# Kernel optimization log

Hardware: AMD Instinct MI355X
Metric: run time of the kernel (lower is better)

The kernel has to match this reference:

```python
import jax, jax.numpy as jnp
import numpy as np

N, F, P, O, E = 20000, 8, 12, 32, 320000


def setup_inputs() -> dict:
    key = jax.random.key(0)
    ks = jax.random.split(key, 18)
    g = lambda k, shape: (jax.random.normal(k, shape, jnp.float32) * 0.1)
    x = jax.random.normal(ks[0], (N, F, P), jnp.float32)
    edge_index = jax.random.randint(ks[1], (2, E), 0, N, dtype=jnp.int32)
    return {
        "x": x,
        "edge_index": edge_index,
        # GCNConv weights/biases for update (z), reset (r), candidate (h) gates
        "Wz": g(ks[2], (F, O)), "bz": g(ks[3], (O,)),
        "Wr": g(ks[4], (F, O)), "br": g(ks[5], (O,)),
        "Wh": g(ks[6], (F, O)), "bh": g(ks[7], (O,)),
        # GRU linear layers (torch.nn.Linear: y = x @ W.T + b), in=2*O, out=O
        "lz_w": g(ks[8], (O, 2 * O)), "lz_b": g(ks[9], (O,)),
        "lr_w": g(ks[10], (O, 2 * O)), "lr_b": g(ks[11], (O,)),
        "lh_w": g(ks[12], (O, 2 * O)), "lh_b": g(ks[13], (O,)),
        # temporal attention logits over periods
        "att": g(ks[14], (P,)),
        # final Linear(32 -> window_size)
        "out_w": g(ks[15], (P, O)), "out_b": g(ks[16], (P,)),
    }


def reference(x, edge_index, Wz, bz, Wr, br, Wh, bh,
              lz_w, lz_b, lr_w, lr_b, lh_w, lh_b, att, out_w, out_b):
    n = x.shape[0]
    # gcn_norm with self-loops: norm_e = d^-1/2[src] * d^-1/2[dst]
    loop = jnp.arange(n, dtype=edge_index.dtype)
    src = jnp.concatenate([edge_index[0], loop])
    dst = jnp.concatenate([edge_index[1], loop])
    deg = jax.ops.segment_sum(jnp.ones(src.shape[0], x.dtype), dst, num_segments=n)
    dinv = jnp.where(deg > 0, deg ** -0.5, 0.0)
    norm = dinv[src] * dinv[dst]  # [E+n]

    def gcn(xp, W, b):
        # xp: [n, P, F] -> [n, P, O]; GCNConv: D^-1/2 (A+I) D^-1/2 (X W) + b
        h = jnp.einsum('npf,fo->npo', xp, W)
        msg = h[src] * norm[:, None, None]  # [E+n, P, O]
        return jax.ops.segment_sum(msg, dst, num_segments=n) + b

    xp = jnp.transpose(x, (0, 2, 1))  # [n, P, F]
    # A3TGCN does NOT carry H across periods (H stays initial zeros), so all
    # periods are independent GRU steps from H = 0 and can be batched.
    H = jnp.zeros(xp.shape[:2] + (O,), x.dtype)
    Z = jax.nn.sigmoid(jnp.concatenate([gcn(xp, Wz, bz), H], -1) @ lz_w.T + lz_b)
    R = jax.nn.sigmoid(jnp.concatenate([gcn(xp, Wr, br), H], -1) @ lr_w.T + lr_b)
    Ht = jnp.tanh(jnp.concatenate([gcn(xp, Wh, bh), H * R], -1) @ lh_w.T + lh_b)
    Hp = Z * H + (1.0 - Z) * Ht  # [n, P, O]
    probs = jax.nn.softmax(att)
    Hacc = jnp.einsum('npo,p->no', Hp, probs)  # attention-weighted sum
    return jax.nn.relu(Hacc) @ out_w.T + out_b  # [n, window_size]
```

## Files before the change

kernel.cpp:

```cpp
#include <hip/hip_runtime.h>
#include <math.h>

#define FP 96
#define SLOT 64
#define NPB 8
#define GBLK 128
#define PBLK 256
#define POISON ((int)0xAAAAAAAA)

__device__ __forceinline__ unsigned f2bf_bits(float f) {
    unsigned u = __float_as_uint(f);
    return (u + 0x7fffu + ((u >> 16) & 1u)) >> 16;
}
__device__ __forceinline__ float bf_lo(unsigned u) { return __uint_as_float(u << 16); }
__device__ __forceinline__ float bf_hi(unsigned u) { return __uint_as_float(u & 0xffff0000u); }

__device__ __forceinline__ int cnt_decode(int v) {
    return ((unsigned)v >= 0xAA000000u) ? v - POISON : v;
}

__global__ void k_hist_fold(const int* __restrict__ ei, int E,
                            int* __restrict__ cnt, int* __restrict__ bucket,
                            const float* __restrict__ Wz, const float* __restrict__ bz,
                            const float* __restrict__ Wh, const float* __restrict__ bh,
                            const float* __restrict__ lz_w, const float* __restrict__ lz_b,
                            const float* __restrict__ lh_w, const float* __restrict__ lh_b,
                            const float* __restrict__ att, const float* __restrict__ out_w,
                            const float* __restrict__ out_b, float* __restrict__ cst) {
    int b = blockIdx.x, t = threadIdx.x;
    if (b == gridDim.x - 1) {
        int f = t >> 5, o = t & 31;
        float sz = 0.f, sh = 0.f;
        for (int j = 0; j < 32; ++j) {
            sz += Wz[f * 32 + j] * lz_w[o * 64 + j];
            sh += Wh[f * 32 + j] * lh_w[o * 64 + j];
        }
        cst[t]       = sz;
        cst[256 + t] = sh;
        if (t < 32) {
            float a = lz_b[t], c = lh_b[t];
            for (int j = 0; j < 32; ++j) {
                a += bz[j] * lz_w[t * 64 + j];
                c += bh[j] * lh_w[t * 64 + j];
            }
            cst[512 + t] = a;
            cst[544 + t] = c;
        }
        if (t < 12) {
            float m = -1e30f;
            for (int p = 0; p < 12; ++p) m = fmaxf(m, att[p]);
            float s = 0.f;
            for (int p = 0; p < 12; ++p) s += expf(att[p] - m);
            cst[576 + t] = expf(att[t] - m) / s;
        }
        for (int i = t; i < 384; i += PBLK)
            cst[588 + (i & 31) * 12 + (i >> 5)] = out_w[i];
        if (t < 12) cst[972 + t] = out_b[t];
        return;
    }
    int e2 = b * PBLK + t;
    int e = e2 << 1;
    if (e >= E) return;
    if (e + 1 < E) {
        int2 s2 = ((const int2*)ei)[e2];
        int2 d2 = ((const int2*)(ei + E))[e2];
        int o0 = atomicAdd(cnt + d2.x, 1);
        int o1 = atomicAdd(cnt + d2.y, 1);
        int p0 = cnt_decode(o0), p1 = cnt_decode(o1);
        if (p0 < SLOT) bucket[(size_t)d2.x * SLOT + p0] = s2.x;
        if (p1 < SLOT) bucket[(size_t)d2.y * SLOT + p1] = s2.y;
    } else {
        int src = ei[e], dst = ei[E + e];
        int old = atomicAdd(cnt + dst, 1);
        int pos = cnt_decode(old);
        if (pos < SLOT) bucket[(size_t)dst * SLOT + pos] = src;
    }
}

__global__ void k_convert(const float* __restrict__ x, const int* __restrict__ cnt,
                          unsigned* __restrict__ xb, int N) {
    int i = blockIdx.x * blockDim.x + threadIdx.x;
    if (i >= (N + 1) * 12) return;
    int n = i / 12;
    if (n == N) {
        ((uint4*)xb)[i] = make_uint4(0u, 0u, 0u, 0u);
        return;
    }
    int deg = cnt_decode(cnt[n]);
    float w = rsqrtf((float)(deg + 1));
    const float4* x4 = (const float4*)x;
    float4 a = x4[i * 2], c = x4[i * 2 + 1];
    uint4 r;
    r.x = f2bf_bits(w * a.x) | (f2bf_bits(w * a.y) << 16);
    r.y = f2bf_bits(w * a.z) | (f2bf_bits(w * a.w) << 16);
    r.z = f2bf_bits(w * c.x) | (f2bf_bits(w * c.y) << 16);
    r.w = f2bf_bits(w * c.z) | (f2bf_bits(w * c.w) << 16);
    ((uint4*)xb)[i] = r;
}

__device__ __forceinline__ void load_batch(uint4* P, const uint4* __restrict__ xrow,
                                           const int* list, int k) {
#pragma unroll
    for (int u = 0; u < 8; ++u) P[u] = xrow[list[u] * 12 + k];
}
__device__ __forceinline__ void acc_batch(float* acc, const uint4* C) {
    acc[0] += ((bf_lo(C[0].x) + bf_lo(C[1].x)) + (bf_lo(C[2].x) + bf_lo(C[3].x)))
            + ((bf_lo(C[4].x) + bf_lo(C[5].x)) + (bf_lo(C[6].x) + bf_lo(C[7].x)));
    acc[1] += ((bf_hi(C[0].x) + bf_hi(C[1].x)) + (bf_hi(C[2].x) + bf_hi(C[3].x)))
            + ((bf_hi(C[4].x) + bf_hi(C[5].x)) + (bf_hi(C[6].x) + bf_hi(C[7].x)));
    acc[2] += ((bf_lo(C[0].y) + bf_lo(C[1].y)) + (bf_lo(C[2].y) + bf_lo(C[3].y)))
            + ((bf_lo(C[4].y) + bf_lo(C[5].y)) + (bf_lo(C[6].y) + bf_lo(C[7].y)));
    acc[3] += ((bf_hi(C[0].y) + bf_hi(C[1].y)) + (bf_hi(C[2].y) + bf_hi(C[3].y)))
            + ((bf_hi(C[4].y) + bf_hi(C[5].y)) + (bf_hi(C[6].y) + bf_hi(C[7].y)));
    acc[4] += ((bf_lo(C[0].z) + bf_lo(C[1].z)) + (bf_lo(C[2].z) + bf_lo(C[3].z)))
            + ((bf_lo(C[4].z) + bf_lo(C[5].z)) + (bf_lo(C[6].z) + bf_lo(C[7].z)));
    acc[5] += ((bf_hi(C[0].z) + bf_hi(C[1].z)) + (bf_hi(C[2].z) + bf_hi(C[3].z)))
            + ((bf_hi(C[4].z) + bf_hi(C[5].z)) + (bf_hi(C[6].z) + bf_hi(C[7].z)));
    acc[6] += ((bf_lo(C[0].w) + bf_lo(C[1].w)) + (bf_lo(C[2].w) + bf_lo(C[3].w)))
            + ((bf_lo(C[4].w) + bf_lo(C[5].w)) + (bf_lo(C[6].w) + bf_lo(C[7].w)));
    acc[7] += ((bf_hi(C[0].w) + bf_hi(C[1].w)) + (bf_hi(C[2].w) + bf_hi(C[3].w)))
            + ((bf_hi(C[4].w) + bf_hi(C[5].w)) + (bf_hi(C[6].w) + bf_hi(C[7].w)));
}

__global__ void __launch_bounds__(GBLK, 4)
k_gather_gates(const unsigned* __restrict__ xb, const int* __restrict__ cnt,
               const int* __restrict__ bucket, const float* __restrict__ cst,
               float* __restrict__ out, int N) {
    __shared__ float sy[NPB][FP + 4];
    __shared__ float shr[NPB][32];
    __shared__ float scst[984];
    __shared__ int   sbuck[NPB][72];
    __shared__ int   sdeg[NPB];
    int t = threadIdx.x;
    int n0 = blockIdx.x * NPB;
    const uint4* xrow = (const uint4*)xb;

    int nl = 0, k = 0, n = N;
    uint4 self = make_uint4(0u, 0u, 0u, 0u);
    if (t < NPB * 12) {
        nl = t / 12; k = t - nl * 12; n = n0 + nl;
        if (n < N) self = xrow[n * 12 + k];
    }
    if (t < NPB) sdeg[t] = (n0 + t < N) ? cnt_decode(cnt[n0 + t]) : 0;
    {
        int nd = t >> 4, q = t & 15, nn = n0 + nd;
        if (nn < N) *(int4*)&sbuck[nd][q * 4] =
            ((const int4*)(bucket + (size_t)nn * SLOT))[q];
    }
    for (int i = t; i < 984; i += GBLK) scst[i] = cst[i];
    __syncthreads();
    if (t < NPB * 8) {
        int nnl = t >> 3, q = t & 7;
        int d = min(sdeg[nnl], SLOT);
        int degp = (d + 7) & ~7; if (degp < 8) degp = 8;
        int pos = d + q;
        if (pos < degp) sbuck[nnl][pos] = N;
    }
    __syncthreads();

    if (t < NPB * 12 && n < N) {
        int c = sdeg[nl];
        int d = min(c, SLOT);
        int degp = (d + 7) & ~7; if (degp < 8) degp = 8;
        int nb = degp >> 3;
        int nA = (nb + 1) >> 1;
        int nB = nb - nA;
        const int* list = sbuck[nl];
        float acc[8] = {bf_lo(self.x), bf_hi(self.x), bf_lo(self.y), bf_hi(self.y),
                        bf_lo(self.z), bf_hi(self.z), bf_lo(self.w), bf_hi(self.w)};
        uint4 A[8], B[8];
        load_batch(A, xrow, list, k);
        if (nB > 0) load_batch(B, xrow, list + nA * 8, k);
        for (int i = 0; i < nA; ++i) {
            acc_batch(acc, A);
            if (i + 1 < nA) load_batch(A, xrow, list + (i + 1) * 8, k);
            if (i < nB) {
                acc_batch(acc, B);
                if (i + 1 < nB) load_batch(B, xrow, list + (nA + i + 1) * 8, k);
            }
        }
        float di = rsqrtf((float)(c + 1));
#pragma unroll
        for (int i = 0; i < 8; ++i) sy[nl][k * 8 + i] = di * acc[i];
    }
    __syncthreads();

    int o = t & 31;
#pragma unroll
    for (int it = 0; it < 2; ++it) {
        int local = (t >> 5) + it * 4, nn = n0 + local;
        if (nn < N) {
            float cz = scst[512 + o], ch = scst[544 + o];
            float hacc = 0.f;
#pragma unroll
            for (int p = 0; p < 12; ++p) {
                float az = cz, ah = ch;
#pragma unroll
                for (int f = 0; f < 8; ++f) {
                    float xf = sy[local][f * 12 + p];
                    az += xf * scst[f * 32 + o];
                    ah += xf * scst[256 + f * 32 + o];
                }
                float ez = __expf(-az);
                float Z  = __builtin_amdgcn_rcpf(1.f + ez);
                float eh = __expf(ah + ah);
                float Ht = 1.f - 2.f * __builtin_amdgcn_rcpf(eh + 1.f);
                hacc += scst[576 + p] * (1.f - Z) * Ht;
            }
            shr[local][o] = fmaxf(hacc, 0.f);
        }
    }
    __syncthreads();
#pragma unroll
    for (int it = 0; it < 2; ++it) {
        int local = (t >> 5) + it * 4, nn = n0 + local;
        if (nn < N && o < 12) {
            float s = scst[972 + o];
#pragma unroll
            for (int j2 = 0; j2 < 32; ++j2)
                s += shr[local][j2] * scst[588 + j2 * 12 + o];
            out[(size_t)nn * 12 + o] = s;
        }
    }
}

extern "C" void kernel_launch(void* const* d_in, const int* in_sizes, int n_in,
                              void* d_out, int out_size, void* d_ws, size_t ws_size,
                              hipStream_t stream) {
    const float* x    = (const float*)d_in[0];
    const int*   ei   = (const int*)d_in[1];
    const float* Wz   = (const float*)d_in[2];
    const float* bz   = (const float*)d_in[3];
    const float* Wh   = (const float*)d_in[6];
    const float* bh   = (const float*)d_in[7];
    const float* lz_w = (const float*)d_in[8];
    const float* lz_b = (const float*)d_in[9];
    const float* lh_w = (const float*)d_in[12];
    const float* lh_b = (const float*)d_in[13];
    const float* att  = (const float*)d_in[14];
    const float* ow   = (const float*)d_in[15];
    const float* ob   = (const float*)d_in[16];
    float* out = (float*)d_out;

    int N = in_sizes[0] / FP;
    int E = in_sizes[1] / 2;

    int*      cnt    = (int*)d_ws;
    int*      bucket = cnt + (N + 1);
    unsigned* xb     = (unsigned*)(bucket + (size_t)N * SLOT);
    float*    cst    = (float*)(xb + (size_t)(N + 1) * 48);

    int EB = (E + PBLK * 2 - 1) / (PBLK * 2);
    k_hist_fold<<<EB + 1, PBLK, 0, stream>>>(ei, E, cnt, bucket, Wz, bz, Wh, bh,
                                             lz_w, lz_b, lh_w, lh_b, att, ow, ob, cst);
    k_convert  <<<((N + 1) * 12 + PBLK - 1) / PBLK, PBLK, 0, stream>>>(x, cnt, xb, N);
    k_gather_gates<<<(N + NPB - 1) / NPB, GBLK, 0, stream>>>(xb, cnt, bucket, cst, out, N);
}
```

Before: 137.0 us.

## Issue first neighbor-row gathers before the barrier, using register-held bucket entries

Each gather thread now reads its node's degree and first 16 bucket indices straight from global memory into registers. It launches the first two 8-neighbor batches of x-row loads before the shared-memory setup barriers, so those loads overlap the block's staging work. The remaining batches go through a single rolling prefetch buffer instead of the previous two-stream A/B interleave. This costs extra registers and redundant bucket reads per thread. The normalization now uses the degree clamped at SLOT, which differs from before only for nodes with more than 64 neighbors.

```diff
diff --git a/kernel.cpp b/kernel.cpp
--- a/kernel.cpp
+++ b/kernel.cpp
@@ -137,49 +137,68 @@
 
     int nl = 0, k = 0, n = N;
     uint4 self = make_uint4(0u, 0u, 0u, 0u);
+    int craw = POISON;
+    int4 b0 = make_int4(N, N, N, N), b1 = b0, b2 = b0, b3 = b0;
     if (t < NPB * 12) {
         nl = t / 12; k = t - nl * 12; n = n0 + nl;
-        if (n < N) self = xrow[n * 12 + k];
+        if (n < N) {
+            self = xrow[n * 12 + k];
+            craw = cnt[n];
+            const int4* bp = (const int4*)(bucket + (size_t)n * SLOT);
+            b0 = bp[0]; b1 = bp[1]; b2 = bp[2]; b3 = bp[3];
+        }
     }
     if (t < NPB) sdeg[t] = (n0 + t < N) ? cnt_decode(cnt[n0 + t]) : 0;
-    {
-        int nd = t >> 4, q = t & 15, nn = n0 + nd;
+    if (t < NPB * 12) {
+        int nd = t / 12, q = 4 + (t - nd * 12), nn = n0 + nd;
         if (nn < N) *(int4*)&sbuck[nd][q * 4] =
             ((const int4*)(bucket + (size_t)nn * SLOT))[q];
     }
     for (int i = t; i < 984; i += GBLK) scst[i] = cst[i];
+
+    int d = 0, nbt = 2;
+    uint4 A[8], B[8];
+    if (t < NPB * 12 && n < N) {
+        int c = cnt_decode(craw);
+        d = min(c, SLOT);
+        nbt = (d <= 16) ? 2 : ((d + 7) >> 3);
+        int l0[8] = { (0 < d) ? b0.x : N, (1 < d) ? b0.y : N,
+                      (2 < d) ? b0.z : N, (3 < d) ? b0.w : N,
+                      (4 < d) ? b1.x : N, (5 < d) ? b1.y : N,
+                      (6 < d) ? b1.z : N, (7 < d) ? b1.w : N };
+        int l1[8] = { (8  < d) ? b2.x : N, (9  < d) ? b2.y : N,
+                      (10 < d) ? b2.z : N, (11 < d) ? b2.w : N,
+                      (12 < d) ? b3.x : N, (13 < d) ? b3.y : N,
+                      (14 < d) ? b3.z : N, (15 < d) ? b3.w : N };
+        load_batch(A, xrow, l0, k);
+        load_batch(B, xrow, l1, k);
+    }
     __syncthreads();
     if (t < NPB * 8) {
         int nnl = t >> 3, q = t & 7;
-        int d = min(sdeg[nnl], SLOT);
-        int degp = (d + 7) & ~7; if (degp < 8) degp = 8;
-        int pos = d + q;
+        int dd = min(sdeg[nnl], SLOT);
+        int degp = (dd + 7) & ~7; if (degp < 8) degp = 8;
+        int pos = dd + q;
         if (pos < degp) sbuck[nnl][pos] = N;
     }
     __syncthreads();
 
     if (t < NPB * 12 && n < N) {
-        int c = sdeg[nl];
-        int d = min(c, SLOT);
-        int degp = (d + 7) & ~7; if (degp < 8) degp = 8;
-        int nb = degp >> 3;
-        int nA = (nb + 1) >> 1;
-        int nB = nb - nA;
         const int* list = sbuck[nl];
         float acc[8] = {bf_lo(self.x), bf_hi(self.x), bf_lo(self.y), bf_hi(self.y),
                         bf_lo(self.z), bf_hi(self.z), bf_lo(self.w), bf_hi(self.w)};
-        uint4 A[8], B[8];
-        load_batch(A, xrow, list, k);
-        if (nB > 0) load_batch(B, xrow, list + nA * 8, k);
-        for (int i = 0; i < nA; ++i) {
-            acc_batch(acc, A);
-            if (i + 1 < nA) load_batch(A, xrow, list + (i + 1) * 8, k);
-            if (i < nB) {
-                acc_batch(acc, B);
-                if (i + 1 < nB) load_batch(B, xrow, list + (nA + i + 1) * 8, k);
-            }
-        }
-        float di = rsqrtf((float)(c + 1));
+        uint4 Ch[8], Cb[8];
+        if (nbt > 2) load_batch(Ch, xrow, list + 16, k);
+        acc_batch(acc, A);
+        acc_batch(acc, B);
+        for (int i = 2; i < nbt; ++i) {
+#pragma unroll
+            for (int u = 0; u < 8; ++u) Cb[u] = Ch[u];
+            if (i + 1 < nbt) load_batch(Ch, xrow, list + (i + 1) * 8, k);
+            acc_batch(acc, Cb);
+        }
+        float di = rsqrtf((float)(min(d, SLOT) == d ? d : d) + 1.f);
+        di = rsqrtf((float)(d + 1));
 #pragma unroll
         for (int i = 0; i < 8; ++i) sy[nl][k * 8 + i] = di * acc[i];
     }
```

Result: slower. 160.2 us (+16.9%).
